# Kernel optimization log

Hardware: AMD Instinct MI355X
Metric: run time of the kernel (lower is better)

## Reference

```python
import jax, jax.numpy as jnp
import numpy as np

RADIUS = 0.1
NSAMPLE = 32
NUM_KP = 15
KP_EXTENT = 1.0
DENSITY_PARAM = 5.0
EXTENT = 2.0 * KP_EXTENT * RADIUS / DENSITY_PARAM  # 0.04
K_RADIUS = 1.5 * EXTENT                            # 0.06
C_IN, C_OUT = 64, 128
BN_EPS = 1e-5


def make_kernel_points():
    # Deterministic stand-in for create_kernel_points: first point at center
    # ('center' fixed mode), remaining points quasi-uniform in a ball of K_RADIUS.
    rs = np.random.RandomState(0)
    d = rs.randn(NUM_KP - 1, 3)
    d /= np.linalg.norm(d, axis=1, keepdims=True) + 1e-9
    r = rs.rand(NUM_KP - 1, 1) ** (1.0 / 3.0)
    pts = np.concatenate([np.zeros((1, 3)), d * r * K_RADIUS], axis=0)
    return jnp.asarray(pts, dtype=jnp.float32)  # [K, 3]


def ball_group(query_xyz, support_xyz, support_mask, radius, nsample):
    """Masked ordered ball query. Returns idx [B,N1,S] int32 and mask [B,N1,S] float."""
    # [B, N1, N2] squared distances (dominant memory traffic)
    d2 = jnp.sum((query_xyz[:, :, None, :] - support_xyz[:, None, :, :]) ** 2, axis=-1)
    valid = (d2 < radius * radius) & (support_mask[:, None, :] > 0)
    order = jnp.cumsum(valid.astype(jnp.int32), axis=-1) - 1  # rank among valid, per row
    in_cap = valid & (order < nsample)
    slot = jnp.where(in_cap, order, nsample)  # overflow -> dump slot
    B, N1, N2 = d2.shape
    j = jnp.broadcast_to(jnp.arange(N2, dtype=jnp.int32), (B, N1, N2))
    b = jnp.arange(B)[:, None, None]
    n = jnp.arange(N1)[None, :, None]
    idx = jnp.zeros((B, N1, nsample + 1), jnp.int32).at[b, n, slot].set(j)[..., :nsample]
    cnt = jnp.sum(in_cap.astype(jnp.int32), axis=-1)  # [B, N1]
    nb_mask = jnp.arange(nsample)[None, None, :] < cnt[:, :, None]
    idx = jnp.where(nb_mask, idx, idx[:, :, :1])  # pad with first neighbor
    return idx, nb_mask.astype(jnp.float32)


def setup_inputs() -> dict:
    key = jax.random.key(0)
    ks = jax.random.split(key, 6)
    B, N1, N2 = 4, 2048, 8192
    query_xyz = jax.random.uniform(ks[0], (B, N1, 3), dtype=jnp.float32)
    support_xyz = jax.random.uniform(ks[1], (B, N2, 3), dtype=jnp.float32)
    query_mask = jnp.ones((B, N1), jnp.float32)
    support_mask = jnp.ones((B, N2), jnp.float32)
    support_features = jax.random.normal(ks[2], (B, C_IN, N2), dtype=jnp.float32)
    kernel_weights = jax.random.normal(ks[3], (NUM_KP, C_IN), dtype=jnp.float32) * (1.0 / np.sqrt(C_IN))
    W_out = jax.random.normal(ks[4], (C_OUT, C_IN), dtype=jnp.float32) * (1.0 / np.sqrt(C_IN))
    gamma = jnp.ones((C_OUT,), jnp.float32)
    beta = jnp.zeros((C_OUT,), jnp.float32)
    return {
        "query_xyz": query_xyz, "support_xyz": support_xyz,
        "query_mask": query_mask, "support_mask": support_mask,
        "support_features": support_features, "K_points": make_kernel_points(),
        "kernel_weights": kernel_weights, "W_out": W_out,
        "gamma": gamma, "beta": beta,
    }


def reference(query_xyz, support_xyz, query_mask, support_mask, support_features,
              K_points, kernel_weights, W_out, gamma, beta):
    idx, nb_mask = ball_group(query_xyz, support_xyz, support_mask, RADIUS, NSAMPLE)
    # gather neighbor features: [B, N2, C] -> [B, N1, S, C]
    feats_t = jnp.transpose(support_features, (0, 2, 1))
    nbr_feats = jnp.take_along_axis(feats_t[:, None, :, :],
                                    idx[:, :, :, None], axis=2)  # [B,N1,S,C]
    # grouped relative positions: [B, N1, S, 3]
    grouped_xyz = jnp.take_along_axis(support_xyz[:, None, :, :],
                                      idx[:, :, :, None], axis=2)
    rel_pos = grouped_xyz - query_xyz[:, :, None, :]
    # kernel-point distances: [B, N1, S, K]
    diff = rel_pos[:, :, :, None, :] - K_points[None, None, None, :, :]
    sq_d = jnp.sum(diff * diff, axis=-1)
    # linear influence, then permute to [B, N1, K, S]
    w = jnp.clip(1.0 - jnp.sqrt(sq_d) / EXTENT, 0.0, None)
    w = jnp.transpose(w, (0, 1, 3, 2))
    feature_mask = nb_mask + (1.0 - query_mask[:, :, None])  # [B,N1,S]
    w = w * feature_mask[:, :, None, :]
    # weighted sum over neighbors: [B, N1, K, C]
    weighted = jnp.einsum('bnks,bnsc->bnkc', w, nbr_feats)
    out = jnp.sum(weighted * kernel_weights[None, None, :, :], axis=2)  # [B,N1,C]
    out = jnp.transpose(out, (0, 2, 1))  # [B, C_in, N1]
    # out_conv: 1x1 conv (no bias) + BatchNorm1d (training-mode batch stats) + ReLU
    out = jnp.einsum('oc,bcn->bon', W_out, out)  # [B, C_out, N1]
    mean = jnp.mean(out, axis=(0, 2), keepdims=True)
    var = jnp.mean((out - mean) ** 2, axis=(0, 2), keepdims=True)
    out = (out - mean) * jax.lax.rsqrt(var + BN_EPS)
    out = out * gamma[None, :, None] + beta[None, :, None]
    return jax.nn.relu(out)
```

## Files before the change

### kernel.cpp

```cpp
#include <hip/hip_runtime.h>
#include <stdint.h>
#include <limits.h>

#define BATCH 4
#define N1D   2048
#define N2D   8192
#define NSAMP 32
#define NKP   15
#define CIN   64
#define COUT  128

#define RAD2    0.01f
#define INV_EXT 25.0f
#define BN_EPS  1e-5f
#define CMARG   0.1000001f

#define QPW   1
#define NWAVE 4
#define QPB   (QPW*NWAVE)
#define NCELL 1000
#define MAXC  96

#define WS_PTS4   0
#define WS_BPTS   131072
#define WS_FEATT  262144
#define WS_WT     2359296
#define WS_OUT2   2367488
#define WS_CS     3416064
#define WS_CNT    3420160
#define WS_CUR    3424256

__device__ __forceinline__ int cell_of(float x, float y, float z) {
  int cx = (int)(x*10.f); cx = cx < 0 ? 0 : (cx > 9 ? 9 : cx);
  int cy = (int)(y*10.f); cy = cy < 0 ? 0 : (cy > 9 ? 9 : cy);
  int cz = (int)(z*10.f); cz = cz < 0 ? 0 : (cz > 9 ? 9 : cz);
  return (cx*10 + cy)*10 + cz;
}

__global__ __launch_bounds__(256) void pg_prep(
    const float* __restrict__ sxyz, const float* __restrict__ smask,
    const float* __restrict__ sfeat, const float* __restrict__ Wout,
    float4* __restrict__ pts4, float* __restrict__ featT, float* __restrict__ Wt,
    int* __restrict__ cellCnt)
{
  __shared__ float tile[64*65];
  const int t  = threadIdx.x;
  const int bt = blockIdx.x;

  if (bt == 512) {
#pragma unroll
    for (int i = 0; i < 32; ++i) {
      const int flat = i*256 + t;
      Wt[flat] = Wout[(flat & 127)*CIN + (flat >> 7)];
    }
    return;
  }

  if (bt >= 513) {
    const int idx = bt - 513;
    const int bb  = idx >> 5;
    const int i   = ((idx & 31) << 8) + t;
    if (smask[bb*N2D + i] > 0.f) {
      const float* p = sxyz + ((size_t)bb*N2D + i)*3;
      atomicAdd(&cellCnt[bb*1024 + cell_of(p[0], p[1], p[2])], 1);
    }
    return;
  }

  const int b  = bt >> 7;
  const int j0 = (bt & 127) * 64;
  if (t < 64) {
    const int g = bt*64 + t;
    pts4[g] = make_float4(sxyz[g*3+0], sxyz[g*3+1], sxyz[g*3+2], 0.f);
  }
  const float* src = sfeat + (size_t)(b*CIN)*N2D + j0;
#pragma unroll
  for (int i = 0; i < 4; ++i) {
    const int c  = i*16 + (t >> 4);
    const int j4 = (t & 15) * 4;
    const float4 v = *(const float4*)(src + (size_t)c*N2D + j4);
    tile[c*65 + j4+0] = v.x;
    tile[c*65 + j4+1] = v.y;
    tile[c*65 + j4+2] = v.z;
    tile[c*65 + j4+3] = v.w;
  }
  __syncthreads();
  float* dstb = featT + (size_t)(b*N2D + j0) * CIN;
#pragma unroll
  for (int r = 0; r < 4; ++r) {
    const int j  = r*16 + (t >> 4);
    const int c4 = (t & 15) * 4;
    float4 v;
    v.x = tile[(c4+0)*65 + j];
    v.y = tile[(c4+1)*65 + j];
    v.z = tile[(c4+2)*65 + j];
    v.w = tile[(c4+3)*65 + j];
    *(float4*)(dstb + j*CIN + c4) = v;
  }
}

__global__ __launch_bounds__(256) void pg_scan(
    const int* __restrict__ cellCnt, int* __restrict__ cellStart,
    int* __restrict__ cellCur)
{
  __shared__ int off_s[NCELL+1];
  __shared__ int wsum[4];
  const int t    = threadIdx.x;
  const int lane = t & 63;
  const int wv   = t >> 6;
  const int bb   = blockIdx.x;
  const int* cnt = cellCnt + bb*1024;

  int c0 = 0, c1 = 0, c2 = 0, c3 = 0, v = 0;
  if (t < 250) {
    c0 = cnt[t*4+0]; c1 = cnt[t*4+1]; c2 = cnt[t*4+2]; c3 = cnt[t*4+3];
    v = c0 + c1 + c2 + c3;
  }
  int x = v;
#pragma unroll
  for (int off = 1; off < 64; off <<= 1) {
    int y = __shfl_up(x, off);
    if (lane >= off) x += y;
  }
  if (lane == 63) wsum[wv] = x;
  __syncthreads();
  int base = 0;
#pragma unroll
  for (int w = 0; w < 4; ++w) if (w < wv) base += wsum[w];
  const int excl = base + x - v;
  if (t < 250) {
    int o = excl;
    off_s[t*4+0] = o; o += c0;
    off_s[t*4+1] = o; o += c1;
    off_s[t*4+2] = o; o += c2;
    off_s[t*4+3] = o;
  }
  if (t == 0) off_s[NCELL] = wsum[0]+wsum[1]+wsum[2]+wsum[3];
  __syncthreads();
  for (int i = t; i < NCELL; i += 256) {
    const int o = off_s[i];
    cellStart[bb*(NCELL+1) + i] = o;
    cellCur[bb*1024 + i] = o;
  }
  if (t == 0) cellStart[bb*(NCELL+1) + NCELL] = off_s[NCELL];
}

__global__ __launch_bounds__(256) void pg_scatter(
    const float* __restrict__ sxyz, const float* __restrict__ smask,
    int* __restrict__ cellCur, float4* __restrict__ bpts)
{
  const int idx = blockIdx.x;
  const int bb  = idx >> 5;
  const int i   = ((idx & 31) << 8) + threadIdx.x;
  if (smask[bb*N2D + i] > 0.f) {
    const float* p = sxyz + ((size_t)bb*N2D + i)*3;
    const float px = p[0], py = p[1], pz = p[2];
    const int pos = atomicAdd(&cellCur[bb*1024 + cell_of(px,py,pz)], 1);
    bpts[(size_t)bb*N2D + pos] = make_float4(px, py, pz, __int_as_float(i));
  }
}

__global__ __launch_bounds__(256) void pg_main(
    const float* __restrict__ qxyz, const float* __restrict__ qmask,
    const float4* __restrict__ pts4, const float4* __restrict__ bpts,
    const int* __restrict__ cellStart, const float* __restrict__ featT,
    const float* __restrict__ Kp, const float* __restrict__ KW,
    const float* __restrict__ Wt, float* __restrict__ out2)
{
  __shared__ int      s_cs[NCELL+1];
  __shared__ int      s_cand[QPB][MAXC];
  __shared__ int      s_idx[QPB*NSAMP];
  __shared__ int      s_cnt[QPB];
  __shared__ float    s_w[QPB*NSAMP*17];
  __shared__ unsigned s_wm[QPB*NSAMP];
  __shared__ float    s_xq[QPB*65];

  const int t    = threadIdx.x;
  const int lane = t & 63;
  const int wv   = t >> 6;
  const int gbase = blockIdx.x * QPB;
  const int b     = gbase >> 11;
  const uint64_t lt = (1ull << lane) - 1ull;

  for (int i = t; i < NCELL+1; i += 256) s_cs[i] = cellStart[b*(NCELL+1) + i];
  __syncthreads();

  const float4* bptsb = bpts + (size_t)b*N2D;
  {
    const int ql = wv;
    const int g  = gbase + ql;
    const float qx = qxyz[g*3+0], qy = qxyz[g*3+1], qz = qxyz[g*3+2];
    int cx0 = (int)((qx-CMARG)*10.f); if (cx0 < 0) cx0 = 0;
    int cx1 = (int)((qx+CMARG)*10.f); if (cx1 > 9) cx1 = 9;
    int cy0 = (int)((qy-CMARG)*10.f); if (cy0 < 0) cy0 = 0;
    int cy1 = (int)((qy+CMARG)*10.f); if (cy1 > 9) cy1 = 9;
    int cz0 = (int)((qz-CMARG)*10.f); if (cz0 < 0) cz0 = 0;
    int cz1 = (int)((qz+CMARG)*10.f); if (cz1 > 9) cz1 = 9;

    int ccnt = 0;
    for (int cx = cx0; cx <= cx1; ++cx) {
      for (int cy = cy0; cy <= cy1; ++cy) {
        const int rowb = (cx*10 + cy)*10;
        const int rs = s_cs[rowb + cz0];
        const int re = s_cs[rowb + cz1 + 1];
        for (int base = rs; base < re; base += 64) {
          const int ii = base + lane;
          bool ok = false; int jj = 0;
          if (ii < re) {
            const float4 p = bptsb[ii];
            const float dx = p.x - qx, dy = p.y - qy, dz = p.z - qz;
            ok = (dx*dx + dy*dy + dz*dz) < RAD2;
            jj = __float_as_int(p.w);
          }
          const uint64_t m = __ballot(ok);
          if (ok) {
            const int pos = ccnt + __popcll(m & lt);
            if (pos < MAXC) s_cand[ql][pos] = jj;
          }
          ccnt += (int)__popcll(m);
        }
      }
    }
    const int C = ccnt < MAXC ? ccnt : MAXC;
    int jA = (lane      < C) ? s_cand[ql][lane]      : INT_MAX;
    int jB = (lane + 64 < C) ? s_cand[ql][lane + 64] : INT_MAX;
    int rA = 0, rB = 0;
    for (int e = 0; e < C; ++e) {
      const int je = s_cand[ql][e];
      rA += (je < jA);
      rB += (je < jB);
    }
    if (lane      < C && rA < NSAMP) s_idx[ql*NSAMP + rA] = jA;
    if (lane + 64 < C && rB < NSAMP) s_idx[ql*NSAMP + rB] = jB;
    if (lane == 0) s_cnt[ql] = C < NSAMP ? C : NSAMP;
  }
  __syncthreads();

  if (t < QPB*NSAMP) {
    const int qslot = t >> 5;
    const int s = t & 31;
    const int c = s_cnt[qslot];
    int j;
    if (s < c) {
      j = s_idx[t];
    } else {
      j = (c > 0) ? s_idx[qslot*NSAMP] : 0;
      s_idx[t] = j;
    }
    const int g = gbase + qslot;
    const float4 pj = pts4[b*N2D + j];
    const float rx = pj.x - qxyz[g*3+0];
    const float ry = pj.y - qxyz[g*3+1];
    const float rz = pj.z - qxyz[g*3+2];

    unsigned msk = 0u;
#pragma unroll
    for (int k = 0; k < NKP; ++k) {
      const float dx = rx - Kp[k*3+0];
      const float dy = ry - Kp[k*3+1];
      const float dz = rz - Kp[k*3+2];
      const float dd = dx*dx + dy*dy + dz*dz;
      const float w = 1.0f - sqrtf(dd) * INV_EXT;
      if (w > 0.0f) {
        s_w[t*17 + k] = w;
        msk |= (1u << k);
      }
    }
    s_wm[t] = msk;
  }
  __syncthreads();

  float kw[NKP];
#pragma unroll
  for (int k = 0; k < NKP; ++k) kw[k] = KW[k*CIN + lane];

  {
    const int ql = wv;
    const int g = gbase + ql;
    const float fpad = 1.0f - qmask[g];
    const int c = __builtin_amdgcn_readfirstlane(s_cnt[ql]);

    float ft[NSAMP];
#pragma unroll
    for (int s = 0; s < NSAMP; ++s) {
      const int j = __builtin_amdgcn_readfirstlane(s_idx[ql*NSAMP + s]);
      ft[s] = featT[(size_t)(b*N2D + j)*CIN + lane];
    }

    float acc = 0.0f;
#pragma unroll
    for (int s = 0; s < NSAMP; ++s) {
      const float fm = ((s < c) ? 1.0f : 0.0f) + fpad;
      if (fm != 0.0f) {
        const unsigned mk =
            (unsigned)__builtin_amdgcn_readfirstlane((int)s_wm[ql*NSAMP + s]);
        if (mk != 0u) {
          const float* wp = &s_w[(ql*NSAMP + s)*17];
          float wsum = 0.0f;
#pragma unroll
          for (int k = 0; k < NKP; ++k)
            if (mk & (1u << k)) wsum += wp[k] * kw[k];
          acc = fmaf(fm*wsum, ft[s], acc);
        }
      }
    }
    s_xq[ql*65 + lane] = acc;
  }
  __syncthreads();

  {
    const int n4 = t & 3;
    const int og = t >> 2;
    const int g  = gbase + n4;
    const int nn = g & 2047;
    float a0 = 0.f, a1 = 0.f;
#pragma unroll
    for (int c = 0; c < CIN; ++c) {
      const float xc = s_xq[n4*65 + c];
      const float2 w2 = *(const float2*)(Wt + c*COUT + og*2);
      a0 = fmaf(w2.x, xc, a0);
      a1 = fmaf(w2.y, xc, a1);
    }
    float* ob = out2 + (size_t)(b*COUT + og*2)*N1D + nn;
    ob[0]   = a0;
    ob[N1D] = a1;
  }
}

__global__ __launch_bounds__(256) void pg_finish(
    const float* __restrict__ out2, const float* __restrict__ gamma,
    const float* __restrict__ beta, float* __restrict__ dout)
{
  __shared__ float red[8];
  __shared__ float mv[2];
  const int t  = threadIdx.x;
  const int o  = blockIdx.x & 127;
  const int bb = blockIdx.x >> 7;
  float4 f[4][2];
  float s1 = 0.f, s2 = 0.f;
#pragma unroll
  for (int r = 0; r < BATCH; ++r) {
    const float4* p = (const float4*)(out2 + (size_t)(r*COUT + o)*N1D);
#pragma unroll
    for (int i = 0; i < 2; ++i) {
      const float4 x = p[i*256 + t];
      f[r][i] = x;
      s1 += x.x + x.y + x.z + x.w;
      s2 += x.x*x.x + x.y*x.y + x.z*x.z + x.w*x.w;
    }
  }
#pragma unroll
  for (int off = 32; off; off >>= 1) {
    s1 += __shfl_xor(s1, off);
    s2 += __shfl_xor(s2, off);
  }
  const int wv = t >> 6;
  if ((t & 63) == 0) { red[wv] = s1; red[4+wv] = s2; }
  __syncthreads();
  if (t == 0) {
    const float inv = 1.0f / (float)(BATCH*N1D);
    const float mean = (red[0]+red[1]+red[2]+red[3]) * inv;
    const float var  = (red[4]+red[5]+red[6]+red[7]) * inv - mean*mean;
    mv[0] = mean;
    mv[1] = rsqrtf(var + BN_EPS);
  }
  __syncthreads();
  const float mean = mv[0];
  const float ga = gamma[o] * mv[1];
  const float be = beta[o];
  float4* dp = (float4*)(dout + (size_t)(bb*COUT + o)*N1D);
#pragma unroll
  for (int i = 0; i < 2; ++i) {
    const float4 x = f[bb][i];
    float4 y;
    y.x = fmaxf((x.x - mean)*ga + be, 0.0f);
    y.y = fmaxf((x.y - mean)*ga + be, 0.0f);
    y.z = fmaxf((x.z - mean)*ga + be, 0.0f);
    y.w = fmaxf((x.w - mean)*ga + be, 0.0f);
    dp[i*256 + t] = y;
  }
}

extern "C" void kernel_launch(void* const* d_in, const int* in_sizes, int n_in,
                              void* d_out, int out_size, void* d_ws, size_t ws_size,
                              hipStream_t stream)
{
  const float* qxyz  = (const float*)d_in[0];
  const float* sxyz  = (const float*)d_in[1];
  const float* qmask = (const float*)d_in[2];
  const float* smask = (const float*)d_in[3];
  const float* sfeat = (const float*)d_in[4];
  const float* Kp    = (const float*)d_in[5];
  const float* KW    = (const float*)d_in[6];
  const float* Wout  = (const float*)d_in[7];
  const float* gamma = (const float*)d_in[8];
  const float* beta  = (const float*)d_in[9];
  float* ws = (float*)d_ws;
  float4* pts4 = (float4*)(ws + WS_PTS4);
  float4* bpts = (float4*)(ws + WS_BPTS);
  float* featT = ws + WS_FEATT;
  float* Wt    = ws + WS_WT;
  float* out2  = ws + WS_OUT2;
  int*   cellS = (int*)(ws + WS_CS);
  int*   cellC = (int*)(ws + WS_CNT);
  int*   cellU = (int*)(ws + WS_CUR);
  float* dst   = (float*)d_out;

  hipMemsetAsync(cellC, 0, BATCH*1024*sizeof(int), stream);
  pg_prep   <<<641,  256, 0, stream>>>(sxyz, smask, sfeat, Wout, pts4, featT,
                                       Wt, cellC);
  pg_scan   <<<4,    256, 0, stream>>>(cellC, cellS, cellU);
  pg_scatter<<<128,  256, 0, stream>>>(sxyz, smask, cellU, bpts);
  pg_main   <<<2048, 256, 0, stream>>>(qxyz, qmask, pts4, bpts, cellS, featT,
                                       Kp, KW, Wt, out2);
  pg_finish <<<512,  256, 0, stream>>>(out2, gamma, beta, dst);
}
```

Baseline: 147.8 us.

## Flatten cell-range scan into single prefix-summed loop and vectorize rank counting

Drops the block-wide copy of the cell-start table into shared memory along with its barrier. Each lane now loads one (x,y) cell row range directly, and a wave prefix-scan builds a flat segment table. The ball-query scan then walks all candidate points in full 64-wide chunks instead of one partially filled chunk per row. The candidate ranking loop reads int4 from shared memory over padded counts. In exchange it adds a per-lane linear segment search and global loads of cellStart per wave.

```diff
diff --git a/kernel.cpp b/kernel.cpp
--- a/kernel.cpp
+++ b/kernel.cpp
@@ -167,7 +167,8 @@
     const float* __restrict__ Kp, const float* __restrict__ KW,
     const float* __restrict__ Wt, float* __restrict__ out2)
 {
-  __shared__ int      s_cs[NCELL+1];
+  __shared__ int      s_segb[QPB][12];
+  __shared__ int      s_segc[QPB][12];
   __shared__ int      s_cand[QPB][MAXC];
   __shared__ int      s_idx[QPB*NSAMP];
   __shared__ int      s_cnt[QPB];
@@ -181,9 +182,6 @@
   const int gbase = blockIdx.x * QPB;
   const int b     = gbase >> 11;
   const uint64_t lt = (1ull << lane) - 1ull;
-
-  for (int i = t; i < NCELL+1; i += 256) s_cs[i] = cellStart[b*(NCELL+1) + i];
-  __syncthreads();
 
   const float4* bptsb = bpts + (size_t)b*N2D;
   {
@@ -196,39 +194,59 @@
     int cy1 = (int)((qy+CMARG)*10.f); if (cy1 > 9) cy1 = 9;
     int cz0 = (int)((qz-CMARG)*10.f); if (cz0 < 0) cz0 = 0;
     int cz1 = (int)((qz+CMARG)*10.f); if (cz1 > 9) cz1 = 9;
+    const int ny = cy1 - cy0 + 1;
+    const int npair = (cx1 - cx0 + 1) * ny;
+
+    int len = 0, rs = 0;
+    if (lane < npair) {
+      const int cx = cx0 + lane / ny;
+      const int cy = cy0 + lane % ny;
+      const int rowb = (cx*10 + cy)*10;
+      const int* csb = cellStart + b*(NCELL+1) + rowb;
+      rs = csb[cz0];
+      len = csb[cz1 + 1] - rs;
+    }
+    int c = len;
+#pragma unroll
+    for (int off = 1; off < 16; off <<= 1) {
+      int y = __shfl_up(c, off);
+      if (lane >= off) c += y;
+    }
+    const int tot = __shfl(c, 15);
+    const int excl = c - len;
+    if (lane < npair) s_segb[ql][lane] = rs - excl;
+    if (lane <= npair) s_segc[ql][lane] = excl;
 
     int ccnt = 0;
-    for (int cx = cx0; cx <= cx1; ++cx) {
-      for (int cy = cy0; cy <= cy1; ++cy) {
-        const int rowb = (cx*10 + cy)*10;
-        const int rs = s_cs[rowb + cz0];
-        const int re = s_cs[rowb + cz1 + 1];
-        for (int base = rs; base < re; base += 64) {
-          const int ii = base + lane;
-          bool ok = false; int jj = 0;
-          if (ii < re) {
-            const float4 p = bptsb[ii];
-            const float dx = p.x - qx, dy = p.y - qy, dz = p.z - qz;
-            ok = (dx*dx + dy*dy + dz*dz) < RAD2;
-            jj = __float_as_int(p.w);
-          }
-          const uint64_t m = __ballot(ok);
-          if (ok) {
-            const int pos = ccnt + __popcll(m & lt);
-            if (pos < MAXC) s_cand[ql][pos] = jj;
-          }
-          ccnt += (int)__popcll(m);
-        }
+    for (int base = 0; base < tot; base += 64) {
+      const int idx = base + lane;
+      bool ok = false; int jj = 0;
+      if (idx < tot) {
+        int p = 0;
+        while (s_segc[ql][p+1] <= idx) ++p;
+        const float4 pt = bptsb[s_segb[ql][p] + idx];
+        const float dx = pt.x - qx, dy = pt.y - qy, dz = pt.z - qz;
+        ok = (dx*dx + dy*dy + dz*dz) < RAD2;
+        jj = __float_as_int(pt.w);
       }
+      const uint64_t m = __ballot(ok);
+      if (ok) {
+        const int pos = ccnt + __popcll(m & lt);
+        if (pos < MAXC) s_cand[ql][pos] = jj;
+      }
+      ccnt += (int)__popcll(m);
     }
     const int C = ccnt < MAXC ? ccnt : MAXC;
+    const int C4 = (C + 3) & ~3;
+    if (C + lane < C4) s_cand[ql][C + lane] = INT_MAX;
+
     int jA = (lane      < C) ? s_cand[ql][lane]      : INT_MAX;
     int jB = (lane + 64 < C) ? s_cand[ql][lane + 64] : INT_MAX;
     int rA = 0, rB = 0;
-    for (int e = 0; e < C; ++e) {
-      const int je = s_cand[ql][e];
-      rA += (je < jA);
-      rB += (je < jB);
+    for (int e = 0; e < C4; e += 4) {
+      const int4 v4 = *(const int4*)&s_cand[ql][e];
+      rA += (v4.x < jA) + (v4.y < jA) + (v4.z < jA) + (v4.w < jA);
+      rB += (v4.x < jB) + (v4.y < jB) + (v4.z < jB) + (v4.w < jB);
     }
     if (lane      < C && rA < NSAMP) s_idx[ql*NSAMP + rA] = jA;
     if (lane + 64 < C && rB < NSAMP) s_idx[ql*NSAMP + rB] = jB;
```

Result: no change. 144.9 us (-1.9%).
